# Performance work log

Hardware: AMD Instinct MI355X
Metric: run time of the kernel (lower is better)

The kernel has to match this reference:

```python
import jax, jax.numpy as jnp
import numpy as np

EPS = 1e-10

def setup_inputs() -> dict:
    key = jax.random.key(0)
    k0, k1, k2, k3, k4, k5 = jax.random.split(key, 6)
    B, S, V, C, D = 256, 20, 20000, 20, 64
    support_set_images = jax.random.uniform(k0, (B, S, V), dtype=jnp.float32)
    support_set_y_one_hot = jax.nn.one_hot(jax.random.randint(k1, (B, S), 0, C), C, dtype=jnp.float32)
    target_image = jax.random.uniform(k2, (B, V), dtype=jnp.float32)
    target_y = jax.random.randint(k3, (B,), 0, C)
    W = jax.random.normal(k4, (D, V), dtype=jnp.float32) * (1.0 / np.sqrt(V).astype(np.float32))
    b = jax.random.normal(k5, (D,), dtype=jnp.float32) * 0.01
    return dict(support_set_images=support_set_images,
                support_set_y_one_hot=support_set_y_one_hot,
                target_image=target_image, target_y=target_y, W=W, b=b)


def reference(support_set_images, support_set_y_one_hot, target_image, target_y, W, b):
    # SentenceEncoder (Linear vocab->64), applied to each support item and the target.
    sup = jnp.einsum('bsv,dv->bsd', support_set_images, W) + b        # [B,S,64]
    tgt = target_image @ W.T + b                                      # [B,64]

    # DistanceNetwork: dot(target, support) * rsqrt(clamp(||support||^2, eps))
    # (only the support vector's magnitude is normalized -- faithful to source).
    mag = jax.lax.rsqrt(jnp.clip(jnp.sum(sup * sup, axis=-1), EPS, None))  # [B,S]
    dots = jnp.einsum('bsd,bd->bs', sup, tgt)                              # [B,S]
    similarities = dots * mag                                              # [B,S]

    # AttentionalClassify: softmax over support, weighted combine of labels.
    attn = jax.nn.softmax(similarities, axis=-1)                           # [B,S]
    preds = jnp.einsum('bs,bsc->bc', attn, support_set_y_one_hot)          # [B,C]

    indices = jnp.argmax(preds, axis=1)
    accuracy = jnp.mean((indices == target_y).astype(jnp.float32))
    # F.cross_entropy applies log_softmax to preds (even though preds are already pdfs).
    logp = jax.nn.log_softmax(preds, axis=-1)
    crossentropy_loss = -jnp.mean(jnp.take_along_axis(logp, target_y[:, None], axis=1))
    return accuracy, crossentropy_loss
```

## Files before the change

kernel.cpp:

```cpp
#include <hip/hip_runtime.h>
#include <hip/hip_bf16.h>
#include <math.h>

#define B_  256
#define S_  20
#define V_  20000
#define C_  20
#define D_  64
#define MTOT (B_*S_ + B_)
#define KSPLIT 10
#define KCHUNK (V_/KSPLIT)
#define KC 80
#define LROW 104
#define MT 64

typedef __bf16 bf16x8 __attribute__((ext_vector_type(8)));
typedef float  f32x4  __attribute__((ext_vector_type(4)));

__device__ __forceinline__ void stage_store(unsigned short* hi, unsigned short* lo,
                                            float4 v) {
    unsigned int ux = __float_as_uint(v.x), uy = __float_as_uint(v.y),
                 uz = __float_as_uint(v.z), uw = __float_as_uint(v.w);
    unsigned int hx = ux & 0xFFFF0000u, hy = uy & 0xFFFF0000u,
                 hz = uz & 0xFFFF0000u, hw = uw & 0xFFFF0000u;
    uint2 h; h.x = (hx >> 16) | hy; h.y = (hz >> 16) | hw;
    *(uint2*)hi = h;
    float rx = v.x - __uint_as_float(hx), ry = v.y - __uint_as_float(hy),
          rz = v.z - __uint_as_float(hz), rw = v.w - __uint_as_float(hw);
    uint2 l;
    l.x = (__float_as_uint(rx) >> 16) | (__float_as_uint(ry) & 0xFFFF0000u);
    l.y = (__float_as_uint(rz) >> 16) | (__float_as_uint(rw) & 0xFFFF0000u);
    *(uint2*)lo = l;
}

__global__ __launch_bounds__(256)
void gemm_mfma_kernel(const float* __restrict__ sup,
                      const float* __restrict__ tgtim,
                      const float* __restrict__ W,
                      float* __restrict__ Ep) {
    __shared__ unsigned short Xhi[MT * LROW], Xlo[MT * LROW];
    __shared__ unsigned short Whi[D_ * LROW], Wlo[D_ * LROW];

    const int bm = blockIdx.x;
    const int bk = blockIdx.y;
    const int t  = threadIdx.x;
    const int w    = t >> 6;
    const int lane = t & 63;
    const int ln = lane & 15;
    const int qd = lane >> 4;
    const int m0 = bm * MT;

    const float* xbase = (m0 < B_*S_)
        ? (sup   + (size_t)m0 * V_)
        : (tgtim + (size_t)(m0 - B_*S_) * V_);

    for (int u = t; u < 4 * 64 * 8; u += 256) {
        const int arr = u >> 9, rem = u & 511;
        const int r = rem >> 3, c = rem & 7;
        unsigned short* base = (arr == 0) ? Xhi : (arr == 1) ? Xlo
                             : (arr == 2) ? Whi : Wlo;
        *(unsigned int*)&base[r * LROW + KC + c * 2] = 0u;
    }

    f32x4 acc[4];
#pragma unroll
    for (int i = 0; i < 4; ++i) acc[i] = (f32x4){0.f, 0.f, 0.f, 0.f};

    const size_t kbase0 = (size_t)bk * KCHUNK;

    for (int ch = 0; ch < KCHUNK / KC; ++ch) {
        const size_t kb = kbase0 + (size_t)ch * KC;
        __syncthreads();
        {
            int u = t;
#pragma unroll
            for (int it = 0; it < 5; ++it, u += 256) {
                const int r = u / 20, c = u % 20;
                const float4 v = *(const float4*)(xbase + (size_t)r * V_ + kb + c * 4);
                stage_store(&Xhi[r * LROW + c * 4], &Xlo[r * LROW + c * 4], v);
            }
            u = t;
#pragma unroll
            for (int it = 0; it < 5; ++it, u += 256) {
                const int r = u / 20, c = u % 20;
                const float4 v = *(const float4*)(W + (size_t)r * V_ + kb + c * 4);
                stage_store(&Whi[r * LROW + c * 4], &Wlo[r * LROW + c * 4], v);
            }
        }
        __syncthreads();

#pragma unroll
        for (int ks = 0; ks < 3; ++ks) {
            const int k0 = ks * 32 + qd * 8;
            const bf16x8 ah = *(const bf16x8*)&Xhi[(16 * w + ln) * LROW + k0];
            const bf16x8 al = *(const bf16x8*)&Xlo[(16 * w + ln) * LROW + k0];
#pragma unroll
            for (int tt = 0; tt < 4; ++tt) {
                const bf16x8 bh = *(const bf16x8*)&Whi[(16 * tt + ln) * LROW + k0];
                const bf16x8 bl = *(const bf16x8*)&Wlo[(16 * tt + ln) * LROW + k0];
                acc[tt] = __builtin_amdgcn_mfma_f32_16x16x32_bf16(ah, bh, acc[tt], 0, 0, 0);
                acc[tt] = __builtin_amdgcn_mfma_f32_16x16x32_bf16(ah, bl, acc[tt], 0, 0, 0);
                acc[tt] = __builtin_amdgcn_mfma_f32_16x16x32_bf16(al, bh, acc[tt], 0, 0, 0);
            }
        }
    }

    const size_t mrow = (size_t)m0 + 16 * w + qd * 4;
#pragma unroll
    for (int tt = 0; tt < 4; ++tt)
#pragma unroll
        for (int r = 0; r < 4; ++r)
            Ep[((size_t)bk * MTOT + mrow + r) * D_ + 16 * tt + ln] = acc[tt][r];
}

__global__ __launch_bounds__(256)
void reduce_kernel(float* __restrict__ Ep) {
    const size_t i = (size_t)blockIdx.x * 256 + threadIdx.x;
    const size_t stride = (size_t)MTOT * D_;
    float4 s = *(const float4*)(Ep + i * 4);
#pragma unroll
    for (int p = 1; p < KSPLIT; ++p) {
        const float4 v = *(const float4*)(Ep + p * stride + i * 4);
        s.x += v.x; s.y += v.y; s.z += v.z; s.w += v.w;
    }
    *(float4*)(Ep + i * 4) = s;
}

__global__ __launch_bounds__(64)
void phase2_kernel(const float* __restrict__ E0,
                   const float* __restrict__ bias,
                   const float* __restrict__ onehot,
                   const int*   __restrict__ ty_,
                   float* __restrict__ res) {
    const int b = blockIdx.x;
    const int d = threadIdx.x;
    const float bv = bias[d];

    float supv[S_];
#pragma unroll
    for (int s = 0; s < S_; ++s)
        supv[s] = E0[((size_t)b * S_ + s) * D_ + d] + bv;
    float tg = E0[((size_t)(B_ * S_) + b) * D_ + d] + bv;

    float sims[S_];
#pragma unroll
    for (int s = 0; s < S_; ++s) {
        float q = supv[s] * supv[s];
        float r = supv[s] * tg;
#pragma unroll
        for (int off = 32; off; off >>= 1) {
            q += __shfl_xor(q, off);
            r += __shfl_xor(r, off);
        }
        sims[s] = r * rsqrtf(fmaxf(q, 1e-10f));
    }

    float mx = sims[0];
#pragma unroll
    for (int s = 1; s < S_; ++s) mx = fmaxf(mx, sims[s]);
    float se = 0.f;
#pragma unroll
    for (int s = 0; s < S_; ++s) { sims[s] = expf(sims[s] - mx); se += sims[s]; }
    const float inv = 1.f / se;

    float pc = -INFINITY;
    if (d < C_) {
        pc = 0.f;
#pragma unroll
        for (int s = 0; s < S_; ++s)
            pc += sims[s] * inv * onehot[((size_t)b * S_ + s) * C_ + d];
    }

    float v = pc;
    int idx = (d < C_) ? d : (1 << 30);
#pragma unroll
    for (int off = 32; off; off >>= 1) {
        const float ov = __shfl_xor(v, off);
        const int   oi = __shfl_xor(idx, off);
        if (ov > v || (ov == v && oi < idx)) { v = ov; idx = oi; }
    }
    float e = (d < C_) ? expf(pc - v) : 0.f;
#pragma unroll
    for (int off = 32; off; off >>= 1) e += __shfl_xor(e, off);
    const float lse = v + logf(e);

    const int ty = ty_[b];
    const float pty = __shfl(pc, ty);

    if (d == 0) {
        res[b]      = (idx == ty) ? 1.f : 0.f;
        res[B_ + b] = lse - pty;
    }
}

__global__ __launch_bounds__(64)
void phase3_kernel(const float* __restrict__ res, float* __restrict__ out) {
    const int t = threadIdx.x;
    float c = 0.f, l = 0.f;
#pragma unroll
    for (int i = 0; i < 4; ++i) {
        c += res[t + 64 * i];
        l += res[B_ + t + 64 * i];
    }
#pragma unroll
    for (int off = 32; off; off >>= 1) {
        c += __shfl_xor(c, off);
        l += __shfl_xor(l, off);
    }
    if (t == 0) {
        out[0] = c * (1.f / 256.f);
        out[1] = l * (1.f / 256.f);
    }
}

extern "C" void kernel_launch(void* const* d_in, const int* in_sizes, int n_in,
                              void* d_out, int out_size, void* d_ws, size_t ws_size,
                              hipStream_t stream) {
    const float* sup    = (const float*)d_in[0];
    const float* onehot = (const float*)d_in[1];
    const float* tgtim  = (const float*)d_in[2];
    const int*   ty     = (const int*)  d_in[3];
    const float* W      = (const float*)d_in[4];
    const float* bias   = (const float*)d_in[5];

    float* Ep  = (float*)d_ws;
    float* res = Ep + (size_t)KSPLIT * MTOT * D_;
    float* out = (float*)d_out;

    gemm_mfma_kernel<<<dim3(MTOT / MT, KSPLIT), 256, 0, stream>>>(sup, tgtim, W, Ep);
    reduce_kernel<<<(MTOT * D_ / 4) / 256, 256, 0, stream>>>(Ep);
    phase2_kernel<<<B_, 64, 0, stream>>>(Ep, bias, onehot, ty, res);
    phase3_kernel<<<1, 64, 0, stream>>>(res, out);
}
```

Measured before the change: 742.5 us.

## Pre-split W into MFMA fragment layout and load operands directly to registers

Adds a kernel that converts W once per call into bf16 hi/lo pairs stored in the MFMA fragment order. The GEMM now drops LDS staging and barriers: each lane loads its X fragment straight from global memory, splits it in registers, and double-buffers both X and W fragments so loads overlap the MFMAs. This removes the shared-memory traffic, the syncs and the repeated per-block W conversion. The cost is uncoalesced strided X row reads, with each lane reading 32 bytes per row, plus one extra kernel launch and extra workspace.

```diff
diff --git a/kernel.cpp b/kernel.cpp
--- a/kernel.cpp
+++ b/kernel.cpp
@@ -9,108 +9,125 @@
 #define D_  64
 #define MTOT (B_*S_ + B_)
 #define KSPLIT 10
-#define KCHUNK (V_/KSPLIT)
-#define KC 80
-#define LROW 104
-#define MT 64
+#define NK32 625
 
 typedef __bf16 bf16x8 __attribute__((ext_vector_type(8)));
 typedef float  f32x4  __attribute__((ext_vector_type(4)));
 
-__device__ __forceinline__ void stage_store(unsigned short* hi, unsigned short* lo,
-                                            float4 v) {
-    unsigned int ux = __float_as_uint(v.x), uy = __float_as_uint(v.y),
-                 uz = __float_as_uint(v.z), uw = __float_as_uint(v.w);
-    unsigned int hx = ux & 0xFFFF0000u, hy = uy & 0xFFFF0000u,
-                 hz = uz & 0xFFFF0000u, hw = uw & 0xFFFF0000u;
-    uint2 h; h.x = (hx >> 16) | hy; h.y = (hz >> 16) | hw;
-    *(uint2*)hi = h;
-    float rx = v.x - __uint_as_float(hx), ry = v.y - __uint_as_float(hy),
-          rz = v.z - __uint_as_float(hz), rw = v.w - __uint_as_float(hw);
-    uint2 l;
-    l.x = (__float_as_uint(rx) >> 16) | (__float_as_uint(ry) & 0xFFFF0000u);
-    l.y = (__float_as_uint(rz) >> 16) | (__float_as_uint(rw) & 0xFFFF0000u);
-    *(uint2*)lo = l;
+__device__ __forceinline__ void split8(const float4 a, const float4 b,
+                                       uint4& hi, uint4& lo) {
+    const float f[8] = {a.x, a.y, a.z, a.w, b.x, b.y, b.z, b.w};
+    unsigned int h[8]; float r[8];
+#pragma unroll
+    for (int j = 0; j < 8; ++j) {
+        const unsigned int u = __float_as_uint(f[j]);
+        h[j] = u & 0xFFFF0000u;
+        r[j] = f[j] - __uint_as_float(h[j]);
+    }
+    hi.x = (h[0] >> 16) | h[1];
+    hi.y = (h[2] >> 16) | h[3];
+    hi.z = (h[4] >> 16) | h[5];
+    hi.w = (h[6] >> 16) | h[7];
+    lo.x = (__float_as_uint(r[0]) >> 16) | (__float_as_uint(r[1]) & 0xFFFF0000u);
+    lo.y = (__float_as_uint(r[2]) >> 16) | (__float_as_uint(r[3]) & 0xFFFF0000u);
+    lo.z = (__float_as_uint(r[4]) >> 16) | (__float_as_uint(r[5]) & 0xFFFF0000u);
+    lo.w = (__float_as_uint(r[6]) >> 16) | (__float_as_uint(r[7]) & 0xFFFF0000u);
 }
 
 __global__ __launch_bounds__(256)
-void gemm_mfma_kernel(const float* __restrict__ sup,
-                      const float* __restrict__ tgtim,
-                      const float* __restrict__ W,
-                      float* __restrict__ Ep) {
-    __shared__ unsigned short Xhi[MT * LROW], Xlo[MT * LROW];
-    __shared__ unsigned short Whi[D_ * LROW], Wlo[D_ * LROW];
-
-    const int bm = blockIdx.x;
-    const int bk = blockIdx.y;
-    const int t  = threadIdx.x;
-    const int w    = t >> 6;
-    const int lane = t & 63;
-    const int ln = lane & 15;
-    const int qd = lane >> 4;
-    const int m0 = bm * MT;
+void wconv_kernel(const float* __restrict__ W,
+                  uint4* __restrict__ Wfh, uint4* __restrict__ Wfl) {
+    const int g    = blockIdx.x * 256 + threadIdx.x;
+    const int lane = g & 63;
+    const int tt   = (g >> 6) & 3;
+    const int c    = g >> 8;
+    const int ln = lane & 15, qd = lane >> 4;
+    const float* src = W + (size_t)(16 * tt + ln) * V_ + c * 32 + qd * 8;
+    const float4 a = *(const float4*)src;
+    const float4 b = *(const float4*)(src + 4);
+    uint4 h, l; split8(a, b, h, l);
+    Wfh[g] = h; Wfl[g] = l;
+}
+
+__device__ __forceinline__ void ldx(const float* xrow, int c, float4& r0, float4& r1) {
+    const float* p = xrow + (size_t)c * 32;
+    r0 = *(const float4*)p;
+    r1 = *(const float4*)(p + 4);
+}
+__device__ __forceinline__ void ldw(const uint4* bh, const uint4* bl, int c,
+                                    uint4* wh, uint4* wl) {
+    const uint4* ph = bh + (size_t)c * 256;
+    const uint4* pl = bl + (size_t)c * 256;
+#pragma unroll
+    for (int tt = 0; tt < 4; ++tt) { wh[tt] = ph[tt * 64]; wl[tt] = pl[tt * 64]; }
+}
+__device__ __forceinline__ void step(const float4 x0, const float4 x1,
+                                     const uint4* wh, const uint4* wl, f32x4* acc) {
+    uint4 hu, lu; split8(x0, x1, hu, lu);
+    const bf16x8 ah = *(const bf16x8*)&hu;
+    const bf16x8 al = *(const bf16x8*)&lu;
+#pragma unroll
+    for (int tt = 0; tt < 4; ++tt) {
+        const bf16x8 bh = *(const bf16x8*)&wh[tt];
+        const bf16x8 bl = *(const bf16x8*)&wl[tt];
+        acc[tt] = __builtin_amdgcn_mfma_f32_16x16x32_bf16(ah, bh, acc[tt], 0, 0, 0);
+        acc[tt] = __builtin_amdgcn_mfma_f32_16x16x32_bf16(ah, bl, acc[tt], 0, 0, 0);
+        acc[tt] = __builtin_amdgcn_mfma_f32_16x16x32_bf16(al, bh, acc[tt], 0, 0, 0);
+    }
+}
+
+__global__ __launch_bounds__(256)
+void gemm2_kernel(const float* __restrict__ sup,
+                  const float* __restrict__ tgtim,
+                  const uint4* __restrict__ Wfh,
+                  const uint4* __restrict__ Wfl,
+                  float* __restrict__ Ep) {
+    const int bmx = blockIdx.x;
+    const int bk  = blockIdx.y;
+    const int t = threadIdx.x;
+    const int w = t >> 6, lane = t & 63;
+    const int ln = lane & 15, qd = lane >> 4;
+    const int m0 = bmx * 64;
 
     const float* xbase = (m0 < B_*S_)
         ? (sup   + (size_t)m0 * V_)
         : (tgtim + (size_t)(m0 - B_*S_) * V_);
-
-    for (int u = t; u < 4 * 64 * 8; u += 256) {
-        const int arr = u >> 9, rem = u & 511;
-        const int r = rem >> 3, c = rem & 7;
-        unsigned short* base = (arr == 0) ? Xhi : (arr == 1) ? Xlo
-                             : (arr == 2) ? Whi : Wlo;
-        *(unsigned int*)&base[r * LROW + KC + c * 2] = 0u;
-    }
+    const float* xrow = xbase + (size_t)(16 * w + ln) * V_ + qd * 8;
+    const uint4* wbh = Wfh + lane;
+    const uint4* wbl = Wfl + lane;
+
+    const int nk = (bk < 5) ? 63 : 62;
+    const int c0 = bk * 62 + ((bk < 5) ? bk : 5);
 
     f32x4 acc[4];
 #pragma unroll
     for (int i = 0; i < 4; ++i) acc[i] = (f32x4){0.f, 0.f, 0.f, 0.f};
 
-    const size_t kbase0 = (size_t)bk * KCHUNK;
-
-    for (int ch = 0; ch < KCHUNK / KC; ++ch) {
-        const size_t kb = kbase0 + (size_t)ch * KC;
-        __syncthreads();
-        {
-            int u = t;
-#pragma unroll
-            for (int it = 0; it < 5; ++it, u += 256) {
-                const int r = u / 20, c = u % 20;
-                const float4 v = *(const float4*)(xbase + (size_t)r * V_ + kb + c * 4);
-                stage_store(&Xhi[r * LROW + c * 4], &Xlo[r * LROW + c * 4], v);
-            }
-            u = t;
-#pragma unroll
-            for (int it = 0; it < 5; ++it, u += 256) {
-                const int r = u / 20, c = u % 20;
-                const float4 v = *(const float4*)(W + (size_t)r * V_ + kb + c * 4);
-                stage_store(&Whi[r * LROW + c * 4], &Wlo[r * LROW + c * 4], v);
-            }
-        }
-        __syncthreads();
-
-#pragma unroll
-        for (int ks = 0; ks < 3; ++ks) {
-            const int k0 = ks * 32 + qd * 8;
-            const bf16x8 ah = *(const bf16x8*)&Xhi[(16 * w + ln) * LROW + k0];
-            const bf16x8 al = *(const bf16x8*)&Xlo[(16 * w + ln) * LROW + k0];
-#pragma unroll
-            for (int tt = 0; tt < 4; ++tt) {
-                const bf16x8 bh = *(const bf16x8*)&Whi[(16 * tt + ln) * LROW + k0];
-                const bf16x8 bl = *(const bf16x8*)&Wlo[(16 * tt + ln) * LROW + k0];
-                acc[tt] = __builtin_amdgcn_mfma_f32_16x16x32_bf16(ah, bh, acc[tt], 0, 0, 0);
-                acc[tt] = __builtin_amdgcn_mfma_f32_16x16x32_bf16(ah, bl, acc[tt], 0, 0, 0);
-                acc[tt] = __builtin_amdgcn_mfma_f32_16x16x32_bf16(al, bh, acc[tt], 0, 0, 0);
-            }
-        }
-    }
-
-    const size_t mrow = (size_t)m0 + 16 * w + qd * 4;
+    float4 xa0, xa1, xc0, xc1;
+    uint4 wha[4], wla[4], whb[4], wlb[4];
+
+    ldx(xrow, c0, xa0, xa1);
+    ldw(wbh, wbl, c0, wha, wla);
+
+    int i = 0;
+    for (; i + 2 <= nk; i += 2) {
+        const int c1 = c0 + i + 1;
+        ldx(xrow, c1, xc0, xc1);
+        ldw(wbh, wbl, c1, whb, wlb);
+        step(xa0, xa1, wha, wla, acc);
+        const int c2 = c0 + ((i + 2 < nk) ? (i + 2) : (i + 1));
+        ldx(xrow, c2, xa0, xa1);
+        ldw(wbh, wbl, c2, wha, wla);
+        step(xc0, xc1, whb, wlb, acc);
+    }
+    if (i < nk) step(xa0, xa1, wha, wla, acc);
+
+    float* dst = Ep + ((size_t)bk * MTOT + m0 + 16 * w + qd * 4) * D_ + ln;
 #pragma unroll
     for (int tt = 0; tt < 4; ++tt)
 #pragma unroll
         for (int r = 0; r < 4; ++r)
-            Ep[((size_t)bk * MTOT + mrow + r) * D_ + 16 * tt + ln] = acc[tt][r];
+            dst[(size_t)r * D_ + 16 * tt] = acc[tt][r];
 }
 
 __global__ __launch_bounds__(256)
@@ -225,9 +242,12 @@
 
     float* Ep  = (float*)d_ws;
     float* res = Ep + (size_t)KSPLIT * MTOT * D_;
+    uint4* Wfh = (uint4*)(res + 512);
+    uint4* Wfl = Wfh + (size_t)NK32 * 4 * 64;
     float* out = (float*)d_out;
 
-    gemm_mfma_kernel<<<dim3(MTOT / MT, KSPLIT), 256, 0, stream>>>(sup, tgtim, W, Ep);
+    wconv_kernel<<<625, 256, 0, stream>>>(W, Wfh, Wfl);
+    gemm2_kernel<<<dim3(84, KSPLIT), 256, 0, stream>>>(sup, tgtim, Wfh, Wfl, Ep);
     reduce_kernel<<<(MTOT * D_ / 4) / 256, 256, 0, stream>>>(Ep);
     phase2_kernel<<<B_, 64, 0, stream>>>(Ep, bias, onehot, ty, res);
     phase3_kernel<<<1, 64, 0, stream>>>(res, out);
```

Result: faster. 666.8 us (-10.2%).
